# Performance work log

Measured on AMD Instinct MI355X. Metric: run time of the kernel, lower is better.

The kernel has to match this reference:

```python
import jax, jax.numpy as jnp
import numpy as np

N = 50000       # nodes
E = 800000      # edges (avg degree 16)
H = 64          # hidden_channels
T = 4           # towers
F = H // T      # per-tower channels (divide_input=True) = 16
NAGG, NSC = 5, 3
# degree histogram passed as mol_deg -> avg log-degree scaler constant (as in PyG PNAConv)
MOL_DEG = np.array([0, 5, 15, 30, 25, 15, 7, 2, 1], dtype=np.float64)
_bins = np.arange(len(MOL_DEG))
AVG_LOG = float((np.log(_bins + 1.0) * MOL_DEG).sum() / MOL_DEG.sum())


def setup_inputs() -> dict:
    key = jax.random.key(0)
    ks = jax.random.split(key, 12)
    g = lambda k, shp, s=0.1: jax.random.normal(k, shp, dtype=jnp.float32) * s
    return {
        "atom_x": g(ks[0], (N, H), 1.0),
        "bond_emb": g(ks[1], (5, H)),                      # Embedding(5, H)
        "edge_w": g(ks[2], (H, F)), "edge_b": jnp.zeros((F,), jnp.float32),
        "pre_w1": g(ks[3], (T, 3 * F, F)), "pre_b1": jnp.zeros((T, F), jnp.float32),
        "pre_w2": g(ks[4], (T, F, F)), "pre_b2": jnp.zeros((T, F), jnp.float32),
        "post_w1": g(ks[5], (T, (1 + NAGG * NSC) * F, F)), "post_b1": jnp.zeros((T, F), jnp.float32),
        "post_w2": g(ks[6], (T, F, F)), "post_b2": jnp.zeros((T, F), jnp.float32),
        "lin_w": g(ks[7], (H, H)), "lin_b": jnp.zeros((H,), jnp.float32),
        "ln_g": jnp.ones((H,), jnp.float32), "ln_b": jnp.zeros((H,), jnp.float32),
        "bond_x": jax.random.randint(ks[8], (E,), 0, 5),
        "atom_edge_index": jax.random.randint(ks[9], (2, E), 0, N),
    }


def reference(atom_x, bond_emb, edge_w, edge_b, pre_w1, pre_b1, pre_w2, pre_b2,
              post_w1, post_b1, post_w2, post_b2, lin_w, lin_b, ln_g, ln_b,
              bond_x, atom_edge_index):
    src, dst = atom_edge_index[0], atom_edge_index[1]
    # bond encoder + PNA edge encoder (edge_dim -> F_in)
    e = bond_emb[bond_x] @ edge_w + edge_b                       # [E, F]
    xt = atom_x.reshape(N, T, F)                                 # divide_input
    x_j, x_i = xt[src], xt[dst]                                  # [E, T, F]
    et = jnp.broadcast_to(e[:, None, :], (E, T, F))
    h = jnp.concatenate([x_i, x_j, et], axis=-1)                 # [E, T, 3F]
    # per-tower pre-MLP (Linear -> ReLU -> Linear)
    h = jax.nn.relu(jnp.einsum('etf,tfg->etg', h, pre_w1) + pre_b1)
    h = jnp.einsum('etf,tfg->etg', h, pre_w2) + pre_b2           # messages [E, T, F]

    s = jax.ops.segment_sum(h, dst, num_segments=N)
    cnt = jax.ops.segment_sum(jnp.ones((E,), h.dtype), dst, num_segments=N)
    cnt_c = jnp.maximum(cnt, 1.0)[:, None, None]
    mean = s / cnt_c
    mean2 = jax.ops.segment_sum(h * h, dst, num_segments=N) / cnt_c
    std = jnp.sqrt(jax.nn.relu(mean2 - mean * mean) + 1e-5)
    has = (cnt > 0)[:, None, None]
    mn = jnp.where(has, jax.ops.segment_min(h, dst, num_segments=N), 0.0)
    mx = jnp.where(has, jax.ops.segment_max(h, dst, num_segments=N), 0.0)
    agg = jnp.concatenate([s, mean, mn, mx, std], axis=-1)       # [N, T, 5F]

    # degree scalers (deg clamped to 1, as in PyG DegreeScalerAggregation)
    ld = jnp.log(jnp.maximum(cnt, 1.0) + 1.0)[:, None, None]
    agg = jnp.concatenate([agg, agg * (ld / AVG_LOG), agg * (AVG_LOG / ld)], axis=-1)  # [N, T, 15F]

    out = jnp.concatenate([xt, agg], axis=-1)                    # [N, T, 16F]
    # per-tower post-MLP, then mix towers with final Linear
    out = jax.nn.relu(jnp.einsum('ntf,tfg->ntg', out, post_w1) + post_b1)
    out = jnp.einsum('ntf,tfg->ntg', out, post_w2) + post_b2     # [N, T, F]
    out = out.reshape(N, H) @ lin_w + lin_b                      # [N, H]

    # LayerNorm + ReLU + residual (dropout is identity in eval)
    mu = out.mean(-1, keepdims=True)
    var = out.var(-1, keepdims=True)
    ln = (out - mu) / jnp.sqrt(var + 1e-5) * ln_g + ln_b
    return atom_x + jax.nn.relu(ln)
```

## Files before the change

### kernel.cpp

```cpp
#include <hip/hip_runtime.h>
#include <cstdint>

typedef unsigned short u16;
typedef _Float16 half4v __attribute__((ext_vector_type(4)));
typedef float f32x4 __attribute__((ext_vector_type(4)));

#define AVG_LOG_F 1.4862356961977451f
#define MAXD 64

#define OFF_W2   3072
#define OFF_PW1  4096
#define OFF_PW2  20480
#define OFF_LW   21504
#define OFF_PB1  25600
#define OFF_PB2  25664
#define OFF_QB1  25728
#define OFF_QB2  25792
#define OFF_LB   25856
#define OFF_LG   25920
#define OFF_LBN  25984
#define OFF_EWT  26128
#define IB       26448

__device__ __forceinline__ float bf2f(u16 u) {
    return __uint_as_float(((unsigned)u) << 16);
}
__device__ __forceinline__ u16 f2bf(float f) {
    unsigned u = __float_as_uint(f);
    u += 0x7fffu + ((u >> 16) & 1u);
    return (u16)(u >> 16);
}
__device__ __forceinline__ float rdin(const void* p, long j, int mode) {
    if (mode == 0) return bf2f(((const u16*)p)[j]);
    return ((const float*)p)[j];
}
template <int MODE>
__device__ __forceinline__ void load16c(const void* p, long base, float* o) {
    if (MODE == 0) {
        const u16* q = (const u16*)p + base;
        uint4 a = *(const uint4*)q;
        uint4 b = *(const uint4*)(q + 8);
        o[0]  = __uint_as_float(a.x << 16); o[1]  = __uint_as_float(a.x & 0xffff0000u);
        o[2]  = __uint_as_float(a.y << 16); o[3]  = __uint_as_float(a.y & 0xffff0000u);
        o[4]  = __uint_as_float(a.z << 16); o[5]  = __uint_as_float(a.z & 0xffff0000u);
        o[6]  = __uint_as_float(a.w << 16); o[7]  = __uint_as_float(a.w & 0xffff0000u);
        o[8]  = __uint_as_float(b.x << 16); o[9]  = __uint_as_float(b.x & 0xffff0000u);
        o[10] = __uint_as_float(b.y << 16); o[11] = __uint_as_float(b.y & 0xffff0000u);
        o[12] = __uint_as_float(b.z << 16); o[13] = __uint_as_float(b.z & 0xffff0000u);
        o[14] = __uint_as_float(b.w << 16); o[15] = __uint_as_float(b.w & 0xffff0000u);
    } else {
        const float* q = (const float*)p + base;
        float4 a = *(const float4*)q;
        float4 b = *(const float4*)(q + 4);
        float4 c = *(const float4*)(q + 8);
        float4 d = *(const float4*)(q + 12);
        o[0]=a.x; o[1]=a.y; o[2]=a.z; o[3]=a.w;
        o[4]=b.x; o[5]=b.y; o[6]=b.z; o[7]=b.w;
        o[8]=c.x; o[9]=c.y; o[10]=c.z; o[11]=c.w;
        o[12]=d.x; o[13]=d.y; o[14]=d.z; o[15]=d.w;
    }
}

template <int MODE>
__device__ __forceinline__ void y_loop(const void* ax, const void* pre_w1, float* wsY, float* wsXW,
                                       int Nn, int wave, int nwaves, int l) {
    const int t = l >> 4, g = l & 15;
    float wxi[16], wxj[16];
#pragma unroll
    for (int f = 0; f < 16; f++) {
        wxi[f] = rdin(pre_w1, t * 768 + f * 16 + g, MODE);
        wxj[f] = rdin(pre_w1, t * 768 + (16 + f) * 16 + g, MODE);
    }
    for (int n = wave; n < Nn; n += nwaves) {
        float xj[16];
        load16c<MODE>(ax, (long)n * 64 + t * 16, xj);
        float accY = 0.f, accX = 0.f;
#pragma unroll
        for (int f = 0; f < 16; f++) {
            accY = fmaf(xj[f], wxj[f], accY);
            accX = fmaf(xj[f], wxi[f], accX);
        }
        wsY[(long)n * 64 + l]  = accY;
        wsXW[(long)n * 64 + l] = accX;
    }
}

__global__ __launch_bounds__(256) void k_prep(
    const int* __restrict__ dstp, const int* __restrict__ srcp, const int* __restrict__ bondp,
    const void* bond_emb, const void* edge_w, const void* edge_b,
    const void* pre_w1, const void* pre_b1, const void* pre_w2, const void* pre_b2,
    const void* post_w1, const void* post_b1, const void* post_w2, const void* post_b2,
    const void* lin_w, const void* lin_b, const void* ln_g, const void* ln_b,
    const void* ax, float* wsf, float* wsY, float* wsXW,
    int* __restrict__ cnt, int* __restrict__ pk, int* modep,
    int Nn, int E, int NIB)
{
    int tid = threadIdx.x;
    if ((int)blockIdx.x >= NIB) {
        int e = ((int)blockIdx.x - NIB) * 256 + tid;
        if (e < E) {
            int d = dstp[e];
            int pos = atomicAdd(&cnt[d], 1);
            if (pos < MAXD) pk[d * MAXD + pos] = (srcp[e] << 9) | (bondp[e] & 7);
        }
        return;
    }
    __shared__ int csh;
    __shared__ float ET[80];
    if (tid == 0) csh = 0;
    __syncthreads();
    {
        unsigned v = ((const unsigned*)ax)[tid];
        unsigned lo = v & 0xffffu;
        int ee = (int)((lo >> 7) & 0xff);
        int isbf = (lo == 0u) || (ee >= 110 && ee <= 140);
        atomicAdd(&csh, isbf);
    }
    __syncthreads();
    int mode = (csh >= 192) ? 0 : 1;

    int b = (int)blockIdx.x;
    int gt = b * 256 + tid;
    int gs = NIB * 256;
    if (b == 0 && tid == 0) modep[0] = mode;

    for (int j = gt; j < 1024; j += gs)  wsf[OFF_W2 + j]  = rdin(pre_w2, j, mode);
    for (int j = gt; j < 16384; j += gs) wsf[OFF_PW1 + j] = rdin(post_w1, j, mode);
    for (int j = gt; j < 1024; j += gs)  wsf[OFF_PW2 + j] = rdin(post_w2, j, mode);
    for (int j = gt; j < 4096; j += gs)  wsf[OFF_LW + j]  = rdin(lin_w, j, mode);
    for (int j = gt; j < 64; j += gs) {
        wsf[OFF_PB1 + j] = rdin(pre_b1, j, mode);
        wsf[OFF_PB2 + j] = rdin(pre_b2, j, mode);
        wsf[OFF_QB1 + j] = rdin(post_b1, j, mode);
        wsf[OFF_QB2 + j] = rdin(post_b2, j, mode);
        wsf[OFF_LB + j]  = rdin(lin_b, j, mode);
        wsf[OFF_LG + j]  = rdin(ln_g, j, mode);
        wsf[OFF_LBN + j] = rdin(ln_b, j, mode);
    }
    if (b == 0) {
        if (tid < 80) {
            int bb = tid >> 4, f = tid & 15;
            float acc = rdin(edge_b, f, mode);
            for (int k = 0; k < 64; k++)
                acc = fmaf(rdin(bond_emb, bb * 64 + k, mode), rdin(edge_w, k * 16 + f, mode), acc);
            ET[tid] = acc;
        }
        __syncthreads();
        for (int j = tid; j < 320; j += 256) {
            int bb = j >> 6, ll = j & 63, tt = ll >> 4, gg = ll & 15;
            float acc = rdin(pre_b1, tt * 16 + gg, mode);
#pragma unroll
            for (int f = 0; f < 16; f++)
                acc = fmaf(ET[bb * 16 + f], rdin(pre_w1, tt * 768 + (32 + f) * 16 + gg, mode), acc);
            wsf[OFF_EWT + j] = acc;
        }
    }
    int wave = gt >> 6;
    int nwaves = gs >> 6;
    int l = tid & 63;
    if (mode == 0) y_loop<0>(ax, pre_w1, wsY, wsXW, Nn, wave, nwaves, l);
    else           y_loop<1>(ax, pre_w1, wsY, wsXW, Nn, wave, nwaves, l);
}

__global__ __launch_bounds__(256, 4) void k_node(
    const void* __restrict__ ax, const float* __restrict__ Yp, const float* __restrict__ XWp,
    const int* __restrict__ pk, const int* __restrict__ cnt,
    const float* __restrict__ wsf, void* __restrict__ outp,
    const int* __restrict__ modep, int Nn)
{
    __shared__ _Float16 hbh[4][16][64];
    __shared__ float    zws[4][5][64];
    __shared__ _Float16 xih[16][64];
    __shared__ _Float16 aggh[5][16][64];
    __shared__ _Float16 p1h[16][64];
    __shared__ _Float16 p2h[16][64];
    __shared__ float    outf[16][64];
    __shared__ float    scl1s[16], scl2s[16];

    const int w = threadIdx.x >> 6;
    const int l = threadIdx.x & 63;
    const int mode = modep[0];

    const int col  = l & 15;
    const int krow = (l >> 4) << 2;

    half4v bfr[4];
    f32x4 cinit[4];
#pragma unroll
    for (int tt = 0; tt < 4; tt++) {
        half4v bv;
#pragma unroll
        for (int i = 0; i < 4; i++)
            bv[i] = (_Float16)wsf[OFF_W2 + tt * 256 + (krow + i) * 16 + col];
        bfr[tt] = bv;
        float pb = wsf[OFF_PB2 + tt * 16 + col];
        cinit[tt] = (f32x4){pb, pb, pb, pb};
    }

    const _Float16* hrow = &hbh[w][col][0];
    const int eswz = (l & 7) << 3;

    for (int j = 0; j < 4; j++) {
        const int ndl = w * 4 + j;
        const int ng  = blockIdx.x * 16 + ndl;
        const bool act = (ng < Nn);
        const int nn = act ? ng : 0;
        int deg = act ? cnt[nn] : 0;
        if (deg > MAXD) deg = MAXD;

        int   pkv = pk[nn * MAXD + l];
        float XWv = XWp[(long)nn * 64 + l];
        zws[w][0][l] = XWv + wsf[OFF_EWT + 0 * 64 + l];
        zws[w][1][l] = XWv + wsf[OFF_EWT + 1 * 64 + l];
        zws[w][2][l] = XWv + wsf[OFF_EWT + 2 * 64 + l];
        zws[w][3][l] = XWv + wsf[OFF_EWT + 3 * 64 + l];
        zws[w][4][l] = XWv + wsf[OFF_EWT + 4 * 64 + l];
        const int nsw = (ndl & 7) << 3;
        xih[ndl][l ^ nsw] = (_Float16)rdin(ax, (long)nn * 64 + l, mode);

        float sA[4]  = {0.f, 0.f, 0.f, 0.f};
        float s2A[4] = {0.f, 0.f, 0.f, 0.f};
        float mnA[4] = {3.0e38f, 3.0e38f, 3.0e38f, 3.0e38f};
        float mxA[4] = {-3.0e38f, -3.0e38f, -3.0e38f, -3.0e38f};

        for (int kb = 0; kb < deg; kb += 16) {
            int B = deg - kb; if (B > 16) B = 16;
            int vs[16]; float yv[16];
#pragma unroll
            for (int k = 0; k < 16; k++) {
                if (k < B) {
                    vs[k] = __builtin_amdgcn_readlane(pkv, kb + k);
                    yv[k] = Yp[(vs[k] >> 3) + l];
                }
            }
#pragma unroll
            for (int k = 0; k < 16; k++) {
                float hv = (k < B) ? fmaxf(yv[k] + zws[w][vs[k] & 7][l], 0.f) : 0.f;
                hbh[w][k][l ^ ((k & 7) << 3)] = (_Float16)hv;
            }
            if (B == 16) {
#pragma unroll
                for (int tt = 0; tt < 4; tt++) {
                    half4v a = *(const half4v*)&hrow[(tt * 16 + krow) ^ eswz];
                    f32x4 d = __builtin_amdgcn_mfma_f32_16x16x16f16(a, bfr[tt], cinit[tt], 0, 0, 0);
#pragma unroll
                    for (int i = 0; i < 4; i++) {
                        float m = d[i];
                        sA[tt] += m;
                        s2A[tt] = fmaf(m, m, s2A[tt]);
                        mnA[tt] = fminf(mnA[tt], m);
                        mxA[tt] = fmaxf(mxA[tt], m);
                    }
                }
            } else {
                const int ebase = kb + krow;
#pragma unroll
                for (int tt = 0; tt < 4; tt++) {
                    half4v a = *(const half4v*)&hrow[(tt * 16 + krow) ^ eswz];
                    f32x4 d = __builtin_amdgcn_mfma_f32_16x16x16f16(a, bfr[tt], cinit[tt], 0, 0, 0);
#pragma unroll
                    for (int i = 0; i < 4; i++) {
                        bool val = (ebase + i) < deg;
                        float m = d[i];
                        float mm = val ? m : 0.f;
                        sA[tt] += mm;
                        s2A[tt] = fmaf(mm, mm, s2A[tt]);
                        mnA[tt] = fminf(mnA[tt], val ? m : 3.0e38f);
                        mxA[tt] = fmaxf(mxA[tt], val ? m : -3.0e38f);
                    }
                }
            }
        }

#pragma unroll
        for (int tt = 0; tt < 4; tt++) {
            sA[tt]  += __shfl_xor(sA[tt], 16);  sA[tt]  += __shfl_xor(sA[tt], 32);
            s2A[tt] += __shfl_xor(s2A[tt], 16); s2A[tt] += __shfl_xor(s2A[tt], 32);
            mnA[tt] = fminf(mnA[tt], __shfl_xor(mnA[tt], 16));
            mnA[tt] = fminf(mnA[tt], __shfl_xor(mnA[tt], 32));
            mxA[tt] = fmaxf(mxA[tt], __shfl_xor(mxA[tt], 16));
            mxA[tt] = fmaxf(mxA[tt], __shfl_xor(mxA[tt], 32));
        }
        const int t = l >> 4;
        float s  = (t & 2) ? ((t & 1) ? sA[3]  : sA[2])  : ((t & 1) ? sA[1]  : sA[0]);
        float s2 = (t & 2) ? ((t & 1) ? s2A[3] : s2A[2]) : ((t & 1) ? s2A[1] : s2A[0]);
        float mn = (t & 2) ? ((t & 1) ? mnA[3] : mnA[2]) : ((t & 1) ? mnA[1] : mnA[0]);
        float mx = (t & 2) ? ((t & 1) ? mxA[3] : mxA[2]) : ((t & 1) ? mxA[1] : mxA[0]);

        if (deg == 0) { mn = 0.f; mx = 0.f; }
        float cf = (float)(deg > 0 ? deg : 1);
        float inv = 1.0f / cf;
        float mean = s * inv;
        float var = s2 * inv - mean * mean;
        float sd = sqrtf(fmaxf(var, 0.f) + 1e-5f);
        float ldv = logf(cf + 1.0f);

        aggh[0][ndl][l ^ nsw] = (_Float16)s;
        aggh[1][ndl][l ^ nsw] = (_Float16)mean;
        aggh[2][ndl][l ^ nsw] = (_Float16)mn;
        aggh[3][ndl][l ^ nsw] = (_Float16)mx;
        aggh[4][ndl][l ^ nsw] = (_Float16)sd;
        if (l == 0) {
            scl1s[ndl] = ldv * (1.0f / AVG_LOG_F);
            scl2s[ndl] = AVG_LOG_F / ldv;
        }
    }
    __syncthreads();

    const int t = w;
    const float* PW1t = wsf + OFF_PW1 + t * 4096;
    const int anode = col;
    const int asw   = (anode & 7) << 3;
    const int achan = t * 16 + krow;

    half4v b1[16];
#pragma unroll
    for (int jj = 0; jj < 16; jj++) {
        int rbase = (jj == 0) ? 0
                  : (jj <= 5)  ? 16  + (jj - 1)  * 16
                  : (jj <= 10) ? 96  + (jj - 6)  * 16
                  :              176 + (jj - 11) * 16;
        half4v bv;
#pragma unroll
        for (int i = 0; i < 4; i++)
            bv[i] = (_Float16)PW1t[(rbase + krow + i) * 16 + col];
        b1[jj] = bv;
    }

    f32x4 zero4 = (f32x4){0.f, 0.f, 0.f, 0.f};
    f32x4 q0, q1v, q2v;
    {
        half4v a = *(const half4v*)&xih[anode][achan ^ asw];
        q0 = __builtin_amdgcn_mfma_f32_16x16x16f16(a, b1[0], zero4, 0, 0, 0);
    }
#pragma unroll
    for (int a5 = 0; a5 < 5; a5++) {
        half4v a = *(const half4v*)&aggh[a5][anode][achan ^ asw];
        q0 = __builtin_amdgcn_mfma_f32_16x16x16f16(a, b1[1 + a5], q0, 0, 0, 0);
    }
    q1v = zero4; q2v = zero4;
#pragma unroll
    for (int a5 = 0; a5 < 5; a5++) {
        half4v a = *(const half4v*)&aggh[a5][anode][achan ^ asw];
        q1v = __builtin_amdgcn_mfma_f32_16x16x16f16(a, b1[6 + a5],  q1v, 0, 0, 0);
        q2v = __builtin_amdgcn_mfma_f32_16x16x16f16(a, b1[11 + a5], q2v, 0, 0, 0);
    }
    {
        float qb1v = wsf[OFF_QB1 + t * 16 + col];
#pragma unroll
        for (int i = 0; i < 4; i++) {
            int ndr = krow + i;
            float p1 = q0[i] + scl1s[ndr] * q1v[i] + scl2s[ndr] * q2v[i] + qb1v;
            p1 = fmaxf(p1, 0.f);
            p1h[ndr][(t * 16 + col) ^ ((ndr & 7) << 3)] = (_Float16)p1;
        }
    }

    {
        const float* PW2t = wsf + OFF_PW2 + t * 256;
        half4v b2;
#pragma unroll
        for (int i = 0; i < 4; i++)
            b2[i] = (_Float16)PW2t[(krow + i) * 16 + col];
        float qb2v = wsf[OFF_QB2 + t * 16 + col];
        f32x4 c2 = (f32x4){qb2v, qb2v, qb2v, qb2v};
        half4v a2 = *(const half4v*)&p1h[anode][achan ^ asw];
        f32x4 m2 = __builtin_amdgcn_mfma_f32_16x16x16f16(a2, b2, c2, 0, 0, 0);
#pragma unroll
        for (int i = 0; i < 4; i++) {
            int ndr = krow + i;
            p2h[ndr][(t * 16 + col) ^ ((ndr & 7) << 3)] = (_Float16)m2[i];
        }
    }
    __syncthreads();

    {
        const float* LWp = wsf + OFF_LW;
        half4v bl[4];
#pragma unroll
        for (int s4 = 0; s4 < 4; s4++) {
            half4v bv;
#pragma unroll
            for (int i = 0; i < 4; i++)
                bv[i] = (_Float16)LWp[(16 * s4 + krow + i) * 64 + 16 * w + col];
            bl[s4] = bv;
        }
        float lbv = wsf[OFF_LB + 16 * w + col];
        f32x4 acc = (f32x4){lbv, lbv, lbv, lbv};
#pragma unroll
        for (int s4 = 0; s4 < 4; s4++) {
            half4v a = *(const half4v*)&p2h[anode][(16 * s4 + krow) ^ asw];
            acc = __builtin_amdgcn_mfma_f32_16x16x16f16(a, bl[s4], acc, 0, 0, 0);
        }
#pragma unroll
        for (int i = 0; i < 4; i++) {
            int ndr = krow + i;
            outf[ndr][16 * w + col] = acc[i];
        }
    }
    __syncthreads();

    for (int j = 0; j < 4; j++) {
        const int ndl = w * 4 + j;
        const int ng  = blockIdx.x * 16 + ndl;
        float a = outf[ndl][l];
        float s1 = a, sq = a * a;
#pragma unroll
        for (int o = 1; o < 64; o <<= 1) { s1 += __shfl_xor(s1, o); sq += __shfl_xor(sq, o); }
        float mu = s1 * (1.0f / 64.0f);
        float varl = sq * (1.0f / 64.0f) - mu * mu;
        float ln = (a - mu) * rsqrtf(varl + 1e-5f) * wsf[OFF_LG + l] + wsf[OFF_LBN + l];
        if (ng < Nn) {
            long idx = (long)ng * 64 + l;
            float res = rdin(ax, idx, mode) + fmaxf(ln, 0.f);
            if (mode == 0) ((u16*)outp)[idx] = f2bf(res);
            else           ((float*)outp)[idx] = res;
        }
    }
}

extern "C" void kernel_launch(void* const* d_in, const int* in_sizes, int n_in,
                              void* d_out, int out_size, void* d_ws, size_t ws_size,
                              hipStream_t stream) {
    const void* atom_x   = d_in[0];
    const void* bond_emb = d_in[1];
    const void* edge_w   = d_in[2];
    const void* edge_b   = d_in[3];
    const void* pre_w1   = d_in[4];
    const void* pre_b1   = d_in[5];
    const void* pre_w2   = d_in[6];
    const void* pre_b2   = d_in[7];
    const void* post_w1  = d_in[8];
    const void* post_b1  = d_in[9];
    const void* post_w2  = d_in[10];
    const void* post_b2  = d_in[11];
    const void* lin_w    = d_in[12];
    const void* lin_b    = d_in[13];
    const void* ln_g     = d_in[14];
    const void* ln_b     = d_in[15];
    const int* bond_x    = (const int*)d_in[16];
    const int* aei       = (const int*)d_in[17];

    int E  = in_sizes[16];
    int Nn = in_sizes[0] / 64;
    const int* srcp = aei;
    const int* dstp = aei + E;

    float* wsf = (float*)d_ws;
    int*   wsi = (int*)d_ws;

    size_t o = IB;
    int* modep = wsi + o; o += 16;
    int* cnt   = wsi + o; o += Nn;
    o = (o + 63) & ~(size_t)63;
    int* pk    = wsi + o; o += (size_t)Nn * MAXD;
    float* Yp  = (float*)(wsi + o); o += (size_t)Nn * 64;
    float* XWp = (float*)(wsi + o); o += (size_t)Nn * 64;

    const int NIB  = 1600;
    const int SBLK = (E + 255) / 256;

    (void)hipMemsetAsync(cnt, 0, (size_t)Nn * sizeof(int), stream);
    k_prep<<<NIB + SBLK, 256, 0, stream>>>(dstp, srcp, bond_x,
                                           bond_emb, edge_w, edge_b,
                                           pre_w1, pre_b1, pre_w2, pre_b2,
                                           post_w1, post_b1, post_w2, post_b2,
                                           lin_w, lin_b, ln_g, ln_b,
                                           atom_x, wsf, Yp, XWp, cnt, pk, modep, Nn, E, NIB);
    dim3 gn((Nn + 15) / 16, 1, 1);
    k_node<<<gn, 256, 0, stream>>>(atom_x, Yp, XWp, pk, cnt, wsf, d_out, modep, Nn);
}
```

Before: 259.9 us.

## Alias LDS buffers, raise occupancy, and prefetch per-node inputs in k_node

Shared-memory use in k_node shrinks by aliasing buffers. outf reuses the zws region, and p1h/p2h reuse slots in aggh. A __syncthreads is added before outf is written so the aliased data is not overwritten too early. The launch bound goes from 4 to 6 blocks per SM, and the four nodes' degree, packed neighbour list, XW and input-row loads are hoisted ahead of the per-node loop so their latency overlaps. The aims are higher occupancy and less exposed global-load latency, at the cost of tighter register limits that may cause spills.

```diff
diff --git a/kernel.cpp b/kernel.cpp
--- a/kernel.cpp
+++ b/kernel.cpp
@@ -162,24 +162,26 @@
     else           y_loop<1>(ax, pre_w1, wsY, wsXW, Nn, wave, nwaves, l);
 }
 
-__global__ __launch_bounds__(256, 4) void k_node(
+__global__ __launch_bounds__(256, 6) void k_node(
     const void* __restrict__ ax, const float* __restrict__ Yp, const float* __restrict__ XWp,
     const int* __restrict__ pk, const int* __restrict__ cnt,
     const float* __restrict__ wsf, void* __restrict__ outp,
     const int* __restrict__ modep, int Nn)
 {
     __shared__ _Float16 hbh[4][16][64];
-    __shared__ float    zws[4][5][64];
+    __shared__ float    zob[1280];
     __shared__ _Float16 xih[16][64];
     __shared__ _Float16 aggh[5][16][64];
-    __shared__ _Float16 p1h[16][64];
-    __shared__ _Float16 p2h[16][64];
-    __shared__ float    outf[16][64];
     __shared__ float    scl1s[16], scl2s[16];
 
     const int w = threadIdx.x >> 6;
     const int l = threadIdx.x & 63;
     const int mode = modep[0];
+
+    float* zws = &zob[w * 320];
+    float (*outf)[64] = (float(*)[64])&zob[0];
+    _Float16 (*p1h)[64] = (_Float16(*)[64])&aggh[0][0][0];
+    _Float16 (*p2h)[64] = (_Float16(*)[64])&aggh[1][0][0];
 
     const int col  = l & 15;
     const int krow = (l >> 4) << 2;
@@ -200,23 +202,33 @@
     const _Float16* hrow = &hbh[w][col][0];
     const int eswz = (l & 7) << 3;
 
+    int pkv4[4]; float XW4[4], xi4[4]; int deg4[4];
+#pragma unroll
+    for (int j = 0; j < 4; j++) {
+        const int ng = blockIdx.x * 16 + w * 4 + j;
+        const bool act = (ng < Nn);
+        const int nn = act ? ng : 0;
+        deg4[j] = act ? cnt[nn] : 0;
+        pkv4[j] = pk[nn * MAXD + l];
+        XW4[j]  = XWp[(long)nn * 64 + l];
+        xi4[j]  = rdin(ax, (long)nn * 64 + l, mode);
+    }
+
+#pragma unroll
     for (int j = 0; j < 4; j++) {
         const int ndl = w * 4 + j;
-        const int ng  = blockIdx.x * 16 + ndl;
-        const bool act = (ng < Nn);
-        const int nn = act ? ng : 0;
-        int deg = act ? cnt[nn] : 0;
+        int deg = deg4[j];
         if (deg > MAXD) deg = MAXD;
-
-        int   pkv = pk[nn * MAXD + l];
-        float XWv = XWp[(long)nn * 64 + l];
-        zws[w][0][l] = XWv + wsf[OFF_EWT + 0 * 64 + l];
-        zws[w][1][l] = XWv + wsf[OFF_EWT + 1 * 64 + l];
-        zws[w][2][l] = XWv + wsf[OFF_EWT + 2 * 64 + l];
-        zws[w][3][l] = XWv + wsf[OFF_EWT + 3 * 64 + l];
-        zws[w][4][l] = XWv + wsf[OFF_EWT + 4 * 64 + l];
+        const int pkv = pkv4[j];
+        const float XWv = XW4[j];
+
+        zws[0 * 64 + l] = XWv + wsf[OFF_EWT + 0 * 64 + l];
+        zws[1 * 64 + l] = XWv + wsf[OFF_EWT + 1 * 64 + l];
+        zws[2 * 64 + l] = XWv + wsf[OFF_EWT + 2 * 64 + l];
+        zws[3 * 64 + l] = XWv + wsf[OFF_EWT + 3 * 64 + l];
+        zws[4 * 64 + l] = XWv + wsf[OFF_EWT + 4 * 64 + l];
         const int nsw = (ndl & 7) << 3;
-        xih[ndl][l ^ nsw] = (_Float16)rdin(ax, (long)nn * 64 + l, mode);
+        xih[ndl][l ^ nsw] = (_Float16)xi4[j];
 
         float sA[4]  = {0.f, 0.f, 0.f, 0.f};
         float s2A[4] = {0.f, 0.f, 0.f, 0.f};
@@ -235,7 +247,7 @@
             }
 #pragma unroll
             for (int k = 0; k < 16; k++) {
-                float hv = (k < B) ? fmaxf(yv[k] + zws[w][vs[k] & 7][l], 0.f) : 0.f;
+                float hv = (k < B) ? fmaxf(yv[k] + zws[(vs[k] & 7) * 64 + l], 0.f) : 0.f;
                 hbh[w][k][l ^ ((k & 7) << 3)] = (_Float16)hv;
             }
             if (B == 16) {
@@ -392,6 +404,7 @@
             half4v a = *(const half4v*)&p2h[anode][(16 * s4 + krow) ^ asw];
             acc = __builtin_amdgcn_mfma_f32_16x16x16f16(a, bl[s4], acc, 0, 0, 0);
         }
+        __syncthreads();
 #pragma unroll
         for (int i = 0; i < 4; i++) {
             int ndr = krow + i;
```

After: 453.3 us. 74.4% more time.
